# Kernel optimization log

Measured on AMD Instinct MI355X. Metric: run time of the kernel, lower is better.

Reference implementation:

```python
import jax, jax.numpy as jnp
import numpy as np

EMBED_DIM = 1024
NUM_HEADS = 16
HEAD_DIM = EMBED_DIM // NUM_HEADS
B, T = 2, 2048


def setup_inputs() -> dict:
    key = jax.random.key(0)
    ks = jax.random.split(key, 5)
    s_in = 1.0 / np.sqrt(EMBED_DIM)
    return {
        "x": jax.random.normal(ks[0], (B, T, EMBED_DIM), dtype=jnp.float32),
        "qkv_w": jax.random.uniform(ks[1], (3 * EMBED_DIM, EMBED_DIM), jnp.float32, -s_in, s_in),
        "qkv_b": jax.random.uniform(ks[2], (3 * EMBED_DIM,), jnp.float32, -s_in, s_in),
        "out_w": jax.random.uniform(ks[3], (EMBED_DIM, EMBED_DIM), jnp.float32, -s_in, s_in),
        "out_b": jax.random.uniform(ks[4], (EMBED_DIM,), jnp.float32, -s_in, s_in),
    }


def reference(x, qkv_w, qkv_b, out_w, out_b):
    b, t, d = x.shape
    scale = HEAD_DIM ** -0.5
    # fused qkv projection: (B, T, 3D)
    qkv = jnp.einsum("btd,ed->bte", x, qkv_w) + qkv_b
    qkv = qkv.reshape(b, t, 3, NUM_HEADS, HEAD_DIM)
    q, k, v = jnp.moveaxis(qkv, 2, 0)  # each (B, T, H, Dh)
    # scores: (B, H, T, T)
    scores = jnp.einsum("bqhd,bkhd->bhqk", q, k) * scale
    attn = jax.nn.softmax(scores, axis=-1)
    # attention output: (B, T, H, Dh) -> (B, T, D)
    ctx = jnp.einsum("bhqk,bkhd->bqhd", attn, v).reshape(b, t, d)
    return jnp.einsum("btd,ed->bte", ctx, out_w) + out_b
```

## Files before the change

### kernel.cpp

```cpp
#include <hip/hip_runtime.h>

typedef __bf16 bf16;
typedef __bf16 bf16x4 __attribute__((ext_vector_type(4)));
typedef __bf16 bf16x8 __attribute__((ext_vector_type(8)));
typedef float f32x4 __attribute__((ext_vector_type(4)));
typedef unsigned int uint2t __attribute__((ext_vector_type(2)));
typedef unsigned int uint4t __attribute__((ext_vector_type(4)));

#define MFMA16(a, b, c) __builtin_amdgcn_mfma_f32_16x16x32_bf16(a, b, c, 0, 0, 0)

__device__ __forceinline__ void lds_load16(void* lds, const void* g) {
  __builtin_amdgcn_global_load_lds(
      (const __attribute__((address_space(1))) unsigned int*)g,
      (__attribute__((address_space(3))) unsigned int*)lds, 16, 0, 0);
}

__global__ void cvt3(const float* __restrict__ x, const float* __restrict__ qw,
                     const float* __restrict__ ow, bf16* __restrict__ xb,
                     bf16* __restrict__ qwb, bf16* __restrict__ owb) {
  const int i = blockIdx.x * blockDim.x + threadIdx.x;
  const float* src;
  bf16* dst;
  int k;
  if (i < 1048576) {
    src = x; dst = xb; k = i;
  } else if (i < 1048576 + 786432) {
    src = qw; dst = qwb; k = i - 1048576;
  } else {
    src = ow; dst = owb; k = i - (1048576 + 786432);
  }
  const float4 v = ((const float4*)src)[k];
  bf16x4 o;
  o[0] = (bf16)v.x; o[1] = (bf16)v.y; o[2] = (bf16)v.z; o[3] = (bf16)v.w;
  ((bf16x4*)dst)[k] = o;
}

__global__ __launch_bounds__(256, 2) void gemm_qkv(
    const bf16* __restrict__ A, const bf16* __restrict__ B,
    const float* __restrict__ bias, bf16* __restrict__ Qb,
    bf16* __restrict__ KF, bf16* __restrict__ VF) {
  const int K = 1024;
  __shared__ bf16 As[128][64];
  __shared__ bf16 Bs[128][64];
  const int tid = threadIdx.x;
  const int w = tid >> 6, lane = tid & 63;
  const int l15 = lane & 15, quad = lane >> 4;
  const int lr = lane >> 3;
  const int lcs = ((lane & 7) ^ lr) * 8;
  const int sw = l15 & 7;
  const int blk = blockIdx.x;
  const int xslot = blk & 7, rest = blk >> 3;
  const int bm = xslot * 4 + (rest & 3);
  const int bn = rest >> 2;
  const int wm = (w >> 1) * 64, wn = (w & 1) * 64;

  const bf16* Abase = A + (size_t)(bm * 128) * K;
  const bf16* Bbase = B + (size_t)(bn * 128) * K;

  f32x4 acc[4][4] = {};

  for (int k0 = 0; k0 < K; k0 += 64) {
#pragma unroll
    for (int c = 0; c < 4; ++c) {
      const int row = w * 32 + c * 8;
      lds_load16(&As[row][0], Abase + (size_t)(row + lr) * K + k0 + lcs);
      lds_load16(&Bs[row][0], Bbase + (size_t)(row + lr) * K + k0 + lcs);
    }
    __syncthreads();
#pragma unroll
    for (int kk = 0; kk < 64; kk += 32) {
      const int cb = kk >> 3;
      bf16x8 am[4], bnf[4];
#pragma unroll
      for (int i = 0; i < 4; ++i)
        am[i] = *(const bf16x8*)&As[wm + i * 16 + l15][((cb + quad) ^ sw) * 8];
#pragma unroll
      for (int j = 0; j < 4; ++j)
        bnf[j] = *(const bf16x8*)&Bs[wn + j * 16 + l15][((cb + quad) ^ sw) * 8];
#pragma unroll
      for (int i = 0; i < 4; ++i)
#pragma unroll
        for (int j = 0; j < 4; ++j)
          acc[i][j] = MFMA16(am[i], bnf[j], acc[i][j]);
    }
    __syncthreads();
  }

#pragma unroll
  for (int j = 0; j < 4; ++j) {
    const int gcol = bn * 128 + wn + j * 16 + l15;
    const float bv = bias[gcol];
#pragma unroll
    for (int i = 0; i < 4; ++i) {
      const int t0 = bm * 128 + wm + i * 16 + quad * 4;
      if (gcol < 1024) {
#pragma unroll
        for (int r = 0; r < 4; ++r)
          Qb[(size_t)(t0 + r) * 1024 + gcol] =
              (bf16)((acc[i][j][r] + bv) * 0.18033688f);
      } else if (gcol < 2048) {
        const int dhl = gcol - 1024;
        const int hh = dhl >> 6, dh = dhl & 63;
        const int tl = t0 & 2047, bb = t0 >> 11;
        const size_t frag = ((size_t)(bb * 16 + hh) * 32 + (tl >> 6)) * 8 +
                            ((tl & 63) >> 4) * 2 + (dh >> 5);
        bf16* p = &KF[frag * 512 +
                      (size_t)(((dh >> 3) & 3) * 16 + (tl & 15)) * 8 + (dh & 7)];
#pragma unroll
        for (int r = 0; r < 4; ++r) p[r * 8] = (bf16)(acc[i][j][r] + bv);
      } else {
        const int dhl = gcol - 2048;
        const int hh = dhl >> 6, dh = dhl & 63;
        const int tl = t0 & 2047, bb = t0 >> 11;
        const size_t frag = ((size_t)(bb * 16 + hh) * 32 + (tl >> 6)) * 8 +
                            (dh >> 4) * 2 + ((tl & 63) >> 5);
        bf16x4 pv;
#pragma unroll
        for (int r = 0; r < 4; ++r) pv[r] = (bf16)(acc[i][j][r] + bv);
        *(bf16x4*)&VF[frag * 512 +
                      (size_t)(((tl & 31) >> 3) * 16 + (dh & 15)) * 8 +
                      (tl & 7)] = pv;
      }
    }
  }
}

__global__ __launch_bounds__(256, 2) void gemm_out(
    const bf16* __restrict__ A, const bf16* __restrict__ B,
    const float* __restrict__ bias, float* __restrict__ Cf) {
  __shared__ bf16 As[64][64];
  __shared__ bf16 Bs[128][64];
  const int tid = threadIdx.x;
  const int w = tid >> 6, lane = tid & 63;
  const int l15 = lane & 15, quad = lane >> 4;
  const int lr = lane >> 3;
  const int lcs = ((lane & 7) ^ lr) * 8;
  const int sw = l15 & 7;
  const int blk = blockIdx.x;
  const int xslot = blk & 7, rest = blk >> 3;
  const int bm = xslot * 8 + (rest & 7);
  const int bn = rest >> 3;

  const bf16* Abase = A + (size_t)(bm * 64) * 1024;
  const bf16* Bbase = B + (size_t)(bn * 128) * 1024;

  f32x4 acc[4][2] = {};

  for (int k0 = 0; k0 < 1024; k0 += 64) {
#pragma unroll
    for (int c = 0; c < 2; ++c) {
      const int row = w * 16 + c * 8;
      lds_load16(&As[row][0], Abase + (size_t)(row + lr) * 1024 + k0 + lcs);
    }
#pragma unroll
    for (int c = 0; c < 4; ++c) {
      const int row = w * 32 + c * 8;
      lds_load16(&Bs[row][0], Bbase + (size_t)(row + lr) * 1024 + k0 + lcs);
    }
    __syncthreads();
#pragma unroll
    for (int kk = 0; kk < 64; kk += 32) {
      const int cb = kk >> 3;
      bf16x8 am[4], bnf[2];
#pragma unroll
      for (int i = 0; i < 4; ++i)
        am[i] = *(const bf16x8*)&As[i * 16 + l15][((cb + quad) ^ sw) * 8];
#pragma unroll
      for (int j = 0; j < 2; ++j)
        bnf[j] =
            *(const bf16x8*)&Bs[w * 32 + j * 16 + l15][((cb + quad) ^ sw) * 8];
#pragma unroll
      for (int i = 0; i < 4; ++i)
#pragma unroll
        for (int j = 0; j < 2; ++j)
          acc[i][j] = MFMA16(am[i], bnf[j], acc[i][j]);
    }
    __syncthreads();
  }

#pragma unroll
  for (int j = 0; j < 2; ++j) {
    const int gcol = bn * 128 + w * 32 + j * 16 + l15;
    const float bv = bias[gcol];
#pragma unroll
    for (int i = 0; i < 4; ++i)
#pragma unroll
      for (int r = 0; r < 4; ++r) {
        const int grow = bm * 64 + i * 16 + quad * 4 + r;
        Cf[(size_t)grow * 1024 + gcol] = acc[i][j][r] + bv;
      }
  }
}

__global__ __launch_bounds__(256, 2) void attn(const bf16* __restrict__ Qb,
                                               const bf16* __restrict__ KF,
                                               const bf16* __restrict__ VF,
                                               bf16* __restrict__ CTX) {
  __shared__ bf16 Kb[2][4096];
  __shared__ bf16 Vb[2][4096];
  const int tid = threadIdx.x, w = tid >> 6, lane = tid & 63;
  const int l15 = lane & 15, quad = lane >> 4;
  const int blk = blockIdx.x;
  const int slot = blk & 7, grp = blk >> 3;
  const int qt = grp & 15, bh = (grp >> 4) * 8 + slot;
  const int h = bh & 15, b = bh >> 4;
  const int q0 = qt * 128;

  const bf16* qrow0 =
      Qb + (size_t)(b * 2048 + q0 + w * 32 + l15) * 1024 + h * 64;
  const bf16* qrow1 = qrow0 + (size_t)16 * 1024;
  const bf16x8 bq0a = *(const bf16x8*)&qrow0[quad * 8];
  const bf16x8 bq0b = *(const bf16x8*)&qrow0[32 + quad * 8];
  const bf16x8 bq1a = *(const bf16x8*)&qrow1[quad * 8];
  const bf16x8 bq1b = *(const bf16x8*)&qrow1[32 + quad * 8];

  const bf16* kfs = KF + (size_t)(b * 16 + h) * 131072;
  const bf16* vfs = VF + (size_t)(b * 16 + h) * 131072;
  const int so = w * 1024;

#pragma unroll
  for (int c = 0; c < 2; ++c) {
    lds_load16(&Kb[0][so + c * 512], kfs + so + c * 512 + lane * 8);
    lds_load16(&Vb[0][so + c * 512], vfs + so + c * 512 + lane * 8);
  }

  float l_run[2] = {0.f, 0.f};
  f32x4 o[2][4] = {};

  for (int kt6 = 0; kt6 < 32; ++kt6) {
    const int cur = kt6 & 1;
    const bf16* kcur = Kb[cur];
    const bf16* vcur = Vb[cur];
    __syncthreads();

    if (kt6 < 31) {
      const size_t nb = (size_t)(kt6 + 1) * 4096;
#pragma unroll
      for (int c = 0; c < 2; ++c) {
        lds_load16(&Kb[cur ^ 1][so + c * 512], kfs + nb + so + c * 512 + lane * 8);
        lds_load16(&Vb[cur ^ 1][so + c * 512], vfs + nb + so + c * 512 + lane * 8);
      }
    }

    f32x4 s[2][4] = {};
#pragma unroll
    for (int k2 = 0; k2 < 2; ++k2)
#pragma unroll
      for (int j = 0; j < 4; ++j) {
        const bf16x8 ak = *(const bf16x8*)&kcur[(j * 2 + k2) * 512 + lane * 8];
        s[0][j] = MFMA16(ak, k2 ? bq0b : bq0a, s[0][j]);
        s[1][j] = MFMA16(ak, k2 ? bq1b : bq1a, s[1][j]);
      }

    bf16x8 bp[2][2];
#pragma unroll
    for (int i = 0; i < 2; ++i) {
      float sum = 0.f;
      uint2t pd[4];
#pragma unroll
      for (int j = 0; j < 4; ++j) {
        bf16x4 pk;
#pragma unroll
        for (int r = 0; r < 4; ++r)
          pk[r] = (bf16)__builtin_amdgcn_exp2f(s[i][j][r]);
#pragma unroll
        for (int r = 0; r < 4; ++r) sum += (float)pk[r];
        pd[j] = __builtin_bit_cast(uint2t, pk);
      }
      l_run[i] += sum;
#pragma unroll
      for (int k2 = 0; k2 < 2; ++k2) {
        uint4t wd;
#pragma unroll
        for (int d = 0; d < 2; ++d) {
          unsigned pa = pd[2 * k2][d], pb = pd[2 * k2 + 1][d];
          asm("v_permlane32_swap_b32 %0, %1" : "+v"(pa), "+v"(pb));
          asm("v_permlane16_swap_b32 %0, %1" : "+v"(pa), "+v"(pb));
          wd[d] = pa;
          wd[2 + d] = pb;
        }
        bp[i][k2] = __builtin_bit_cast(bf16x8, wd);
      }
    }

#pragma unroll
    for (int k2 = 0; k2 < 2; ++k2)
#pragma unroll
      for (int j = 0; j < 4; ++j) {
        const bf16x8 av = *(const bf16x8*)&vcur[(j * 2 + k2) * 512 + lane * 8];
        o[0][j] = MFMA16(av, bp[0][k2], o[0][j]);
        o[1][j] = MFMA16(av, bp[1][k2], o[1][j]);
      }
  }

#pragma unroll
  for (int i = 0; i < 2; ++i) {
    l_run[i] += __shfl_xor(l_run[i], 16);
    l_run[i] += __shfl_xor(l_run[i], 32);
  }

#pragma unroll
  for (int i = 0; i < 2; ++i) {
    const float inv = 1.f / l_run[i];
    bf16* crow =
        CTX + (size_t)(b * 2048 + q0 + w * 32 + i * 16 + l15) * 1024 + h * 64;
#pragma unroll
    for (int j = 0; j < 4; ++j) {
      bf16x4 ov;
#pragma unroll
      for (int r = 0; r < 4; ++r) ov[r] = (bf16)(o[i][j][r] * inv);
      *(bf16x4*)&crow[j * 16 + quad * 4] = ov;
    }
  }
}

extern "C" void kernel_launch(void* const* d_in, const int* in_sizes, int n_in,
                              void* d_out, int out_size, void* d_ws,
                              size_t ws_size, hipStream_t stream) {
  const float* x = (const float*)d_in[0];
  const float* qkv_w = (const float*)d_in[1];
  const float* qkv_b = (const float*)d_in[2];
  const float* out_w = (const float*)d_in[3];
  const float* out_b = (const float*)d_in[4];
  float* out = (float*)d_out;

  bf16* xb = (bf16*)d_ws;
  bf16* wqkv = xb + (size_t)4096 * 1024;
  bf16* wout = wqkv + (size_t)3072 * 1024;
  bf16* qb = wout + (size_t)1024 * 1024;
  bf16* kf = qb + (size_t)4096 * 1024;
  bf16* vf = kf + (size_t)4096 * 1024;
  bf16* ctx = vf + (size_t)4096 * 1024;

  cvt3<<<2097152 / 256, 256, 0, stream>>>(x, qkv_w, out_w, xb, wqkv, wout);

  gemm_qkv<<<768, 256, 0, stream>>>(xb, wqkv, qkv_b, qb, kf, vf);
  attn<<<512, 256, 0, stream>>>(qb, kf, vf, ctx);
  gemm_out<<<512, 256, 0, stream>>>(ctx, wout, out_b, out);
}
```

Baseline: 186.3 us.

## Split attention KV range across two wave groups and use fp16 for PV path

The attention kernel grows to 512 threads: two groups of four waves each handle half of the key/value sequence for the same query tile. Their partial outputs and row sums are merged through LDS at the end. V, the softmax probabilities, the context and the output weight switch from bf16 to fp16 with fp16 MFMA, which gives the probabilities more mantissa bits. The split doubles the waves working in parallel on the serial KV loop, at the cost of an extra LDS reduction and more register pressure under launch bounds of 4 blocks.

```diff
diff --git a/kernel.cpp b/kernel.cpp
--- a/kernel.cpp
+++ b/kernel.cpp
@@ -3,11 +3,15 @@
 typedef __bf16 bf16;
 typedef __bf16 bf16x4 __attribute__((ext_vector_type(4)));
 typedef __bf16 bf16x8 __attribute__((ext_vector_type(8)));
+typedef _Float16 f16;
+typedef _Float16 f16x4 __attribute__((ext_vector_type(4)));
+typedef _Float16 f16x8 __attribute__((ext_vector_type(8)));
 typedef float f32x4 __attribute__((ext_vector_type(4)));
 typedef unsigned int uint2t __attribute__((ext_vector_type(2)));
 typedef unsigned int uint4t __attribute__((ext_vector_type(4)));
 
 #define MFMA16(a, b, c) __builtin_amdgcn_mfma_f32_16x16x32_bf16(a, b, c, 0, 0, 0)
+#define MFMA16F(a, b, c) __builtin_amdgcn_mfma_f32_16x16x32_f16(a, b, c, 0, 0, 0)
 
 __device__ __forceinline__ void lds_load16(void* lds, const void* g) {
   __builtin_amdgcn_global_load_lds(
@@ -17,28 +21,34 @@
 
 __global__ void cvt3(const float* __restrict__ x, const float* __restrict__ qw,
                      const float* __restrict__ ow, bf16* __restrict__ xb,
-                     bf16* __restrict__ qwb, bf16* __restrict__ owb) {
+                     bf16* __restrict__ qwb, f16* __restrict__ owb) {
   const int i = blockIdx.x * blockDim.x + threadIdx.x;
-  const float* src;
-  bf16* dst;
-  int k;
-  if (i < 1048576) {
-    src = x; dst = xb; k = i;
-  } else if (i < 1048576 + 786432) {
-    src = qw; dst = qwb; k = i - 1048576;
+  if (i < 1048576 + 786432) {
+    const float* src;
+    bf16* dst;
+    int k;
+    if (i < 1048576) {
+      src = x; dst = xb; k = i;
+    } else {
+      src = qw; dst = qwb; k = i - 1048576;
+    }
+    const float4 v = ((const float4*)src)[k];
+    bf16x4 o;
+    o[0] = (bf16)v.x; o[1] = (bf16)v.y; o[2] = (bf16)v.z; o[3] = (bf16)v.w;
+    ((bf16x4*)dst)[k] = o;
   } else {
-    src = ow; dst = owb; k = i - (1048576 + 786432);
-  }
-  const float4 v = ((const float4*)src)[k];
-  bf16x4 o;
-  o[0] = (bf16)v.x; o[1] = (bf16)v.y; o[2] = (bf16)v.z; o[3] = (bf16)v.w;
-  ((bf16x4*)dst)[k] = o;
+    const int k = i - (1048576 + 786432);
+    const float4 v = ((const float4*)ow)[k];
+    f16x4 o;
+    o[0] = (f16)v.x; o[1] = (f16)v.y; o[2] = (f16)v.z; o[3] = (f16)v.w;
+    ((f16x4*)owb)[k] = o;
+  }
 }
 
 __global__ __launch_bounds__(256, 2) void gemm_qkv(
     const bf16* __restrict__ A, const bf16* __restrict__ B,
     const float* __restrict__ bias, bf16* __restrict__ Qb,
-    bf16* __restrict__ KF, bf16* __restrict__ VF) {
+    bf16* __restrict__ KF, f16* __restrict__ VF) {
   const int K = 1024;
   __shared__ bf16 As[128][64];
   __shared__ bf16 Bs[128][64];
@@ -114,22 +124,22 @@
         const int tl = t0 & 2047, bb = t0 >> 11;
         const size_t frag = ((size_t)(bb * 16 + hh) * 32 + (tl >> 6)) * 8 +
                             (dh >> 4) * 2 + ((tl & 63) >> 5);
-        bf16x4 pv;
-#pragma unroll
-        for (int r = 0; r < 4; ++r) pv[r] = (bf16)(acc[i][j][r] + bv);
-        *(bf16x4*)&VF[frag * 512 +
-                      (size_t)(((tl & 31) >> 3) * 16 + (dh & 15)) * 8 +
-                      (tl & 7)] = pv;
+        f16x4 pv;
+#pragma unroll
+        for (int r = 0; r < 4; ++r) pv[r] = (f16)(acc[i][j][r] + bv);
+        *(f16x4*)&VF[frag * 512 +
+                     (size_t)(((tl & 31) >> 3) * 16 + (dh & 15)) * 8 +
+                     (tl & 7)] = pv;
       }
     }
   }
 }
 
 __global__ __launch_bounds__(256, 2) void gemm_out(
-    const bf16* __restrict__ A, const bf16* __restrict__ B,
+    const f16* __restrict__ A, const f16* __restrict__ B,
     const float* __restrict__ bias, float* __restrict__ Cf) {
-  __shared__ bf16 As[64][64];
-  __shared__ bf16 Bs[128][64];
+  __shared__ f16 As[64][64];
+  __shared__ f16 Bs[128][64];
   const int tid = threadIdx.x;
   const int w = tid >> 6, lane = tid & 63;
   const int l15 = lane & 15, quad = lane >> 4;
@@ -141,8 +151,8 @@
   const int bm = xslot * 8 + (rest & 7);
   const int bn = rest >> 3;
 
-  const bf16* Abase = A + (size_t)(bm * 64) * 1024;
-  const bf16* Bbase = B + (size_t)(bn * 128) * 1024;
+  const f16* Abase = A + (size_t)(bm * 64) * 1024;
+  const f16* Bbase = B + (size_t)(bn * 128) * 1024;
 
   f32x4 acc[4][2] = {};
 
@@ -161,19 +171,19 @@
 #pragma unroll
     for (int kk = 0; kk < 64; kk += 32) {
       const int cb = kk >> 3;
-      bf16x8 am[4], bnf[2];
+      f16x8 am[4], bnf[2];
 #pragma unroll
       for (int i = 0; i < 4; ++i)
-        am[i] = *(const bf16x8*)&As[i * 16 + l15][((cb + quad) ^ sw) * 8];
+        am[i] = *(const f16x8*)&As[i * 16 + l15][((cb + quad) ^ sw) * 8];
 #pragma unroll
       for (int j = 0; j < 2; ++j)
         bnf[j] =
-            *(const bf16x8*)&Bs[w * 32 + j * 16 + l15][((cb + quad) ^ sw) * 8];
+            *(const f16x8*)&Bs[w * 32 + j * 16 + l15][((cb + quad) ^ sw) * 8];
 #pragma unroll
       for (int i = 0; i < 4; ++i)
 #pragma unroll
         for (int j = 0; j < 2; ++j)
-          acc[i][j] = MFMA16(am[i], bnf[j], acc[i][j]);
+          acc[i][j] = MFMA16F(am[i], bnf[j], acc[i][j]);
     }
     __syncthreads();
   }
@@ -192,13 +202,13 @@
   }
 }
 
-__global__ __launch_bounds__(256, 2) void attn(const bf16* __restrict__ Qb,
+__global__ __launch_bounds__(512, 4) void attn(const bf16* __restrict__ Qb,
                                                const bf16* __restrict__ KF,
-                                               const bf16* __restrict__ VF,
-                                               bf16* __restrict__ CTX) {
-  __shared__ bf16 Kb[2][4096];
-  __shared__ bf16 Vb[2][4096];
+                                               const f16* __restrict__ VF,
+                                               f16* __restrict__ CTX) {
+  __shared__ bf16 KV[2][2][2][4096];
   const int tid = threadIdx.x, w = tid >> 6, lane = tid & 63;
+  const int g = w >> 2, wg = w & 3;
   const int l15 = lane & 15, quad = lane >> 4;
   const int blk = blockIdx.x;
   const int slot = blk & 7, grp = blk >> 3;
@@ -207,38 +217,40 @@
   const int q0 = qt * 128;
 
   const bf16* qrow0 =
-      Qb + (size_t)(b * 2048 + q0 + w * 32 + l15) * 1024 + h * 64;
+      Qb + (size_t)(b * 2048 + q0 + wg * 32 + l15) * 1024 + h * 64;
   const bf16* qrow1 = qrow0 + (size_t)16 * 1024;
   const bf16x8 bq0a = *(const bf16x8*)&qrow0[quad * 8];
   const bf16x8 bq0b = *(const bf16x8*)&qrow0[32 + quad * 8];
   const bf16x8 bq1a = *(const bf16x8*)&qrow1[quad * 8];
   const bf16x8 bq1b = *(const bf16x8*)&qrow1[32 + quad * 8];
 
-  const bf16* kfs = KF + (size_t)(b * 16 + h) * 131072;
-  const bf16* vfs = VF + (size_t)(b * 16 + h) * 131072;
-  const int so = w * 1024;
+  const bf16* kfs = KF + (size_t)(b * 16 + h) * 131072 + (size_t)g * 65536;
+  const f16* vfs = VF + (size_t)(b * 16 + h) * 131072 + (size_t)g * 65536;
+  const int so = wg * 1024;
 
 #pragma unroll
   for (int c = 0; c < 2; ++c) {
-    lds_load16(&Kb[0][so + c * 512], kfs + so + c * 512 + lane * 8);
-    lds_load16(&Vb[0][so + c * 512], vfs + so + c * 512 + lane * 8);
+    lds_load16(&KV[g][0][0][so + c * 512], kfs + so + c * 512 + lane * 8);
+    lds_load16(&KV[g][1][0][so + c * 512], vfs + so + c * 512 + lane * 8);
   }
 
   float l_run[2] = {0.f, 0.f};
   f32x4 o[2][4] = {};
 
-  for (int kt6 = 0; kt6 < 32; ++kt6) {
-    const int cur = kt6 & 1;
-    const bf16* kcur = Kb[cur];
-    const bf16* vcur = Vb[cur];
-    __syncthreads();
-
-    if (kt6 < 31) {
-      const size_t nb = (size_t)(kt6 + 1) * 4096;
+  for (int kt = 0; kt < 16; ++kt) {
+    const int cur = kt & 1;
+    const bf16* kcur = &KV[g][0][cur][0];
+    const f16* vcur = (const f16*)&KV[g][1][cur][0];
+    __syncthreads();
+
+    if (kt < 15) {
+      const size_t nb = (size_t)(kt + 1) * 4096;
 #pragma unroll
       for (int c = 0; c < 2; ++c) {
-        lds_load16(&Kb[cur ^ 1][so + c * 512], kfs + nb + so + c * 512 + lane * 8);
-        lds_load16(&Vb[cur ^ 1][so + c * 512], vfs + nb + so + c * 512 + lane * 8);
+        lds_load16(&KV[g][0][cur ^ 1][so + c * 512],
+                   kfs + nb + so + c * 512 + lane * 8);
+        lds_load16(&KV[g][1][cur ^ 1][so + c * 512],
+                   vfs + nb + so + c * 512 + lane * 8);
       }
     }
 
@@ -252,17 +264,17 @@
         s[1][j] = MFMA16(ak, k2 ? bq1b : bq1a, s[1][j]);
       }
 
-    bf16x8 bp[2][2];
+    f16x8 bp[2][2];
 #pragma unroll
     for (int i = 0; i < 2; ++i) {
       float sum = 0.f;
       uint2t pd[4];
 #pragma unroll
       for (int j = 0; j < 4; ++j) {
-        bf16x4 pk;
+        f16x4 pk;
 #pragma unroll
         for (int r = 0; r < 4; ++r)
-          pk[r] = (bf16)__builtin_amdgcn_exp2f(s[i][j][r]);
+          pk[r] = (f16)__builtin_amdgcn_exp2f(s[i][j][r]);
 #pragma unroll
         for (int r = 0; r < 4; ++r) sum += (float)pk[r];
         pd[j] = __builtin_bit_cast(uint2t, pk);
@@ -279,7 +291,7 @@
           wd[d] = pa;
           wd[2 + d] = pb;
         }
-        bp[i][k2] = __builtin_bit_cast(bf16x8, wd);
+        bp[i][k2] = __builtin_bit_cast(f16x8, wd);
       }
     }
 
@@ -287,9 +299,9 @@
     for (int k2 = 0; k2 < 2; ++k2)
 #pragma unroll
       for (int j = 0; j < 4; ++j) {
-        const bf16x8 av = *(const bf16x8*)&vcur[(j * 2 + k2) * 512 + lane * 8];
-        o[0][j] = MFMA16(av, bp[0][k2], o[0][j]);
-        o[1][j] = MFMA16(av, bp[1][k2], o[1][j]);
+        const f16x8 av = *(const f16x8*)&vcur[(j * 2 + k2) * 512 + lane * 8];
+        o[0][j] = MFMA16F(av, bp[0][k2], o[0][j]);
+        o[1][j] = MFMA16F(av, bp[1][k2], o[1][j]);
       }
   }
 
@@ -299,17 +311,34 @@
     l_run[i] += __shfl_xor(l_run[i], 32);
   }
 
-#pragma unroll
-  for (int i = 0; i < 2; ++i) {
-    const float inv = 1.f / l_run[i];
-    bf16* crow =
-        CTX + (size_t)(b * 2048 + q0 + w * 32 + i * 16 + l15) * 1024 + h * 64;
-#pragma unroll
-    for (int j = 0; j < 4; ++j) {
-      bf16x4 ov;
-#pragma unroll
-      for (int r = 0; r < 4; ++r) ov[r] = (bf16)(o[i][j][r] * inv);
-      *(bf16x4*)&crow[j * 16 + quad * 4] = ov;
+  __syncthreads();
+  float* ob = (float*)&KV[0][0][0][0];
+  float* lb = ob + 128 * 68;
+  if (g == 1) {
+#pragma unroll
+    for (int i = 0; i < 2; ++i) {
+      const int q = wg * 32 + i * 16 + l15;
+#pragma unroll
+      for (int j = 0; j < 4; ++j)
+        *(f32x4*)&ob[q * 68 + j * 16 + quad * 4] = o[i][j];
+      if (quad == 0) lb[q] = l_run[i];
+    }
+  }
+  __syncthreads();
+  if (g == 0) {
+#pragma unroll
+    for (int i = 0; i < 2; ++i) {
+      const int q = wg * 32 + i * 16 + l15;
+      const float inv = 1.f / (l_run[i] + lb[q]);
+      f16* crow = CTX + (size_t)(b * 2048 + q0 + q) * 1024 + h * 64;
+#pragma unroll
+      for (int j = 0; j < 4; ++j) {
+        const f32x4 ox = o[i][j] + *(const f32x4*)&ob[q * 68 + j * 16 + quad * 4];
+        f16x4 ov;
+#pragma unroll
+        for (int r = 0; r < 4; ++r) ov[r] = (f16)(ox[r] * inv);
+        *(f16x4*)&crow[j * 16 + quad * 4] = ov;
+      }
     }
   }
 }
@@ -324,17 +353,18 @@
   const float* out_b = (const float*)d_in[4];
   float* out = (float*)d_out;
 
-  bf16* xb = (bf16*)d_ws;
-  bf16* wqkv = xb + (size_t)4096 * 1024;
-  bf16* wout = wqkv + (size_t)3072 * 1024;
-  bf16* qb = wout + (size_t)1024 * 1024;
-  bf16* kf = qb + (size_t)4096 * 1024;
-  bf16* vf = kf + (size_t)4096 * 1024;
-  bf16* ctx = vf + (size_t)4096 * 1024;
+  bf16* base = (bf16*)d_ws;
+  bf16* xb = base;
+  bf16* wqkv = base + (size_t)4096 * 1024;
+  f16* wout = (f16*)(base + (size_t)7168 * 1024);
+  bf16* qb = base + (size_t)8192 * 1024;
+  bf16* kf = base + (size_t)12288 * 1024;
+  f16* vf = (f16*)(base + (size_t)16384 * 1024);
+  f16* ctx = (f16*)(base + (size_t)20480 * 1024);
 
   cvt3<<<2097152 / 256, 256, 0, stream>>>(x, qkv_w, out_w, xb, wqkv, wout);
 
   gemm_qkv<<<768, 256, 0, stream>>>(xb, wqkv, qkv_b, qb, kf, vf);
-  attn<<<512, 256, 0, stream>>>(qb, kf, vf, ctx);
+  attn<<<512, 512, 0, stream>>>(qb, kf, vf, ctx);
   gemm_out<<<512, 256, 0, stream>>>(ctx, wout, out_b, out);
 }
```

Measured after the change: 178.8 us. 1.04x faster.
